# Kernel tuning notes

Hardware: AMD Instinct MI355X
Metric: run time of the kernel (lower is better)

Reference implementation:

```python
import jax, jax.numpy as jnp
import numpy as np

VOCAB, EMB, HID = 32000, 128, 128
B, S = 8, 1024


def setup_inputs() -> dict:
    key = jax.random.key(0)
    ks = jax.random.split(key, 8)
    scale_e = 1.0  # nn.Embedding default N(0,1)
    k_rnn = 1.0 / np.sqrt(HID)  # nn.RNN uniform(-1/sqrt(H), 1/sqrt(H))
    k_fc = 1.0 / np.sqrt(HID)
    return {
        "x": jax.random.randint(ks[0], (B, S), 0, VOCAB),
        "emb_table": jax.random.normal(ks[1], (VOCAB, EMB), dtype=jnp.float32) * scale_e,
        "W_ih": jax.random.uniform(ks[2], (HID, EMB), jnp.float32, -k_rnn, k_rnn),
        "b_ih": jax.random.uniform(ks[3], (HID,), jnp.float32, -k_rnn, k_rnn),
        "W_hh": jax.random.uniform(ks[4], (HID, HID), jnp.float32, -k_rnn, k_rnn),
        "b_hh": jax.random.uniform(ks[5], (HID,), jnp.float32, -k_rnn, k_rnn),
        "fc_W": jax.random.uniform(ks[6], (VOCAB, HID), jnp.float32, -k_fc, k_fc),
        "fc_b": jax.random.uniform(ks[7], (VOCAB,), jnp.float32, -k_fc, k_fc),
    }


def reference(x, emb_table, W_ih, b_ih, W_hh, b_hh, fc_W, fc_b):
    # Embedding lookup: [B,S,E]
    e = emb_table[x]
    # Precompute input projection for all timesteps: [B,S,H]
    x_proj = jnp.einsum("bse,he->bsh", e, W_ih) + b_ih + b_hh

    h0 = jnp.zeros((x.shape[0], W_hh.shape[0]), dtype=e.dtype)

    def step(h, xp_t):  # xp_t: [B,H]
        h_new = jnp.tanh(xp_t + h @ W_hh.T)
        return h_new, h_new

    # scan over time: xs [S,B,H]
    h_last, hs = jax.lax.scan(step, h0, jnp.swapaxes(x_proj, 0, 1))
    outputs = jnp.swapaxes(hs, 0, 1)  # [B,S,H]
    logits = jnp.einsum("bsh,vh->bsv", outputs, fc_W) + fc_b  # [B,S,V]
    hidden_state = h_last[None]  # [1,B,H] matching torch num_layers dim
    return logits, hidden_state
```

## Files before the change

kernel.cpp:

```cpp
#include <hip/hip_runtime.h>
#include <hip/hip_bf16.h>

#define VOCAB 32000
#define EMB   128
#define HID   128
#define BB    8
#define SS    1024

typedef __bf16 bf16x8_t __attribute__((ext_vector_type(8)));
typedef float  f32x4_t  __attribute__((ext_vector_type(4)));

__device__ __forceinline__ float dpp_xor1(float x) {
    return __int_as_float(__builtin_amdgcn_update_dpp(
        0, __float_as_int(x), 0xB1, 0xF, 0xF, true));
}
__device__ __forceinline__ float dpp_xor2(float x) {
    return __int_as_float(__builtin_amdgcn_update_dpp(
        0, __float_as_int(x), 0x4E, 0xF, 0xF, true));
}

__global__ __launch_bounds__(512) void xproj_kernel(
    const int* __restrict__ x, const float* __restrict__ emb,
    const float* __restrict__ W_ih, const float* __restrict__ b_ih,
    const float* __restrict__ b_hh, float* __restrict__ xp)
{
    const int t  = threadIdx.x;
    const int h  = t >> 2;
    const int ks = t & 3;

    float w[32];
    {
        const float* wr = W_ih + h * EMB + ks * 32;
        #pragma unroll
        for (int i = 0; i < 32; i += 4) {
            float4 v = *(const float4*)(wr + i);
            w[i] = v.x; w[i+1] = v.y; w[i+2] = v.z; w[i+3] = v.w;
        }
    }
    const float bias = b_ih[h] + b_hh[h];

    __shared__ float el[2][EMB];
    const int base = blockIdx.x * 32;

    float4 v = make_float4(0.f, 0.f, 0.f, 0.f);
    if (t < 32) v = *(const float4*)(emb + (size_t)x[base] * EMB + t * 4);

    for (int r = 0; r < 32; ++r) {
        if (t < 32) *(float4*)(&el[r & 1][t * 4]) = v;
        __syncthreads();
        if (t < 32 && r + 1 < 32)
            v = *(const float4*)(emb + (size_t)x[base + r + 1] * EMB + t * 4);

        float a0 = 0.f, a1 = 0.f, a2 = 0.f, a3 = 0.f;
        const float* e = &el[r & 1][ks * 32];
        #pragma unroll
        for (int c = 0; c < 8; ++c) {
            float4 hv = *(const float4*)(e + c * 4);
            a0 = fmaf(w[c*4+0], hv.x, a0);
            a1 = fmaf(w[c*4+1], hv.y, a1);
            a2 = fmaf(w[c*4+2], hv.z, a2);
            a3 = fmaf(w[c*4+3], hv.w, a3);
        }
        float sum = (a0 + a1) + (a2 + a3);
        sum += __shfl_xor(sum, 1);
        sum += __shfl_xor(sum, 2);
        if (ks == 0) xp[(size_t)(base + r) * HID + h] = bias + sum;
    }
}

__global__ __launch_bounds__(256) void convert_bf16_kernel(
    const float* __restrict__ in, __hip_bfloat16* __restrict__ out)
{
    const size_t i = ((size_t)blockIdx.x * 256 + threadIdx.x) * 8;
    float4 a = *(const float4*)(in + i);
    float4 b = *(const float4*)(in + i + 4);
    union { __hip_bfloat16 h[8]; uint4 u; } p;
    p.h[0] = __float2bfloat16(a.x); p.h[1] = __float2bfloat16(a.y);
    p.h[2] = __float2bfloat16(a.z); p.h[3] = __float2bfloat16(a.w);
    p.h[4] = __float2bfloat16(b.x); p.h[5] = __float2bfloat16(b.y);
    p.h[6] = __float2bfloat16(b.z); p.h[7] = __float2bfloat16(b.w);
    *(uint4*)(out + i) = p.u;
}

__global__ __launch_bounds__(256) void mega_kernel(
    const float* __restrict__ xp, const float* __restrict__ W_hh,
    __hip_bfloat16* __restrict__ hs_bf16, float* __restrict__ hidden_out,
    const __hip_bfloat16* __restrict__ Wb, const float* __restrict__ fc_b,
    float* __restrict__ C, unsigned int* __restrict__ prog)
{
    const int bid = blockIdx.x;

    if (bid < BB) {
        const int b  = bid;
        const int t  = threadIdx.x;
        const int w  = t >> 6;
        const int l  = t & 63;
        const int ks = l & 3;
        const int g  = l >> 2;
        const int jb = w * 16 + g;

        f32x4_t wr[2][8];
        #pragma unroll
        for (int m = 0; m < 2; ++m) {
            const float* src = W_hh + (size_t)(jb + 64 * m) * HID + ks * 32;
            #pragma unroll
            for (int i = 0; i < 8; ++i) wr[m][i] = *(const f32x4_t*)(src + i * 4);
        }

        __shared__ float hbuf[2][160];
        if (t < 160) hbuf[0][t] = 0.f;

        const float* xpb = xp + (size_t)b * SS * HID;
        const bool  wrt  = (ks == 0);
        const int rbase = ks * 40;

        float xsA[8][2], xsB[8][2];
        if (wrt) {
            #pragma unroll
            for (int u = 0; u < 8; ++u) {
                xsA[u][0] = xpb[(size_t)u * HID + jb];
                xsA[u][1] = xpb[(size_t)u * HID + jb + 64];
            }
        }
        __syncthreads();

#define RNN_SUPERSTEP(XC, XN, BASE)                                          \
    {                                                                        \
        const int nbase_ = (BASE) + 8;                                       \
        if (wrt && nbase_ < SS) {                                            \
            _Pragma("unroll")                                                \
            for (int u = 0; u < 8; ++u) {                                    \
                XN[u][0] = xpb[(size_t)(nbase_ + u) * HID + jb];             \
                XN[u][1] = xpb[(size_t)(nbase_ + u) * HID + jb + 64];        \
            }                                                                \
        }                                                                    \
        _Pragma("unroll")                                                    \
        for (int u = 0; u < 8; ++u) {                                        \
            const int step_ = (BASE) + u;                                    \
            const float* hc_ = hbuf[u & 1];                                  \
            f32x4_t hv[8];                                                   \
            _Pragma("unroll")                                                \
            for (int i = 0; i < 4; ++i)                                      \
                hv[i] = *(const f32x4_t*)(hc_ + rbase + i * 4);              \
            _Pragma("unroll")                                                \
            for (int i = 4; i < 8; ++i)                                      \
                hv[i] = *(const f32x4_t*)(hc_ + rbase + 4 + i * 4);          \
            f32x4_t a0 = {0.f,0.f,0.f,0.f}, a1 = a0, c0 = a0, c1 = a0;       \
            _Pragma("unroll")                                                \
            for (int i = 0; i < 4; ++i) {                                    \
                a0 += wr[0][i]   * hv[i];                                    \
                a1 += wr[0][i+4] * hv[i+4];                                  \
                c0 += wr[1][i]   * hv[i];                                    \
                c1 += wr[1][i+4] * hv[i+4];                                  \
            }                                                                \
            f32x4_t av = a0 + a1, cv = c0 + c1;                              \
            float s0 = (av.x + av.y) + (av.z + av.w);                        \
            float s1 = (cv.x + cv.y) + (cv.z + cv.w);                        \
            s0 += dpp_xor1(s0);  s0 += dpp_xor2(s0);                         \
            s1 += dpp_xor1(s1);  s1 += dpp_xor2(s1);                         \
            if (wrt) {                                                       \
                const float z0 = XC[u][0] + s0;                              \
                const float e0 = __expf(2.0f * z0);                          \
                const float h0 = 1.0f - 2.0f * __builtin_amdgcn_rcpf(e0 + 1.0f); \
                const float z1 = XC[u][1] + s1;                              \
                const float e1 = __expf(2.0f * z1);                          \
                const float h1 = 1.0f - 2.0f * __builtin_amdgcn_rcpf(e1 + 1.0f); \
                const int j0 = jb, j1 = jb + 64;                             \
                hbuf[(u + 1) & 1][j0 + ((j0 >> 4) << 2)] = h0;               \
                hbuf[(u + 1) & 1][j1 + ((j1 >> 4) << 2)] = h1;               \
                hs_bf16[((size_t)b * SS + step_) * HID + j0] = __float2bfloat16(h0); \
                hs_bf16[((size_t)b * SS + step_) * HID + j1] = __float2bfloat16(h1); \
                if (step_ == SS - 1) {                                       \
                    hidden_out[b * HID + j0] = h0;                           \
                    hidden_out[b * HID + j1] = h1;                           \
                }                                                            \
            }                                                                \
            asm volatile("s_waitcnt lgkmcnt(0)" ::: "memory");               \
            __builtin_amdgcn_s_barrier();                                    \
        }                                                                    \
    }

        for (int chunk = 0; chunk < 8; ++chunk) {
            for (int sb2 = 0; sb2 < 8; ++sb2) {
                const int base = chunk * 128 + sb2 * 16;
                RNN_SUPERSTEP(xsA, xsB, base);
                RNN_SUPERSTEP(xsB, xsA, base + 8);
            }
            asm volatile("s_waitcnt vmcnt(0)" ::: "memory");
            __builtin_amdgcn_s_barrier();
            if (t == 0)
                __hip_atomic_store(&prog[b * 16], (unsigned)(chunk + 1),
                                   __ATOMIC_RELEASE, __HIP_MEMORY_SCOPE_AGENT);
        }
#undef RNN_SUPERSTEP
    } else {
        const int cid  = bid - BB;
        const int NC   = 256 - BB;
        const int t    = threadIdx.x;
        const int lane = t & 63;
        const int cw   = t >> 6;
        const int wm   = cw >> 1;
        const int wn   = cw & 1;
        const int lr   = lane & 15;
        const int kq   = lane >> 4;

        for (int tc = 0; tc < 8; ++tc) {
            if (t == 0) {
                for (int b2 = 0; b2 < BB; ++b2) {
                    while (__hip_atomic_fetch_add(&prog[b2 * 16], 0u,
                               __ATOMIC_RELAXED, __HIP_MEMORY_SCOPE_AGENT)
                           < (unsigned)(tc + 1))
                        __builtin_amdgcn_s_sleep(32);
                }
            }
            __syncthreads();
            __builtin_amdgcn_fence(__ATOMIC_ACQUIRE, "agent");

            for (int i = cid; i < 2000; i += NC) {
                const int b2 = i / 250;
                const int nb = i % 250;
                const int mb = b2 * 8 + tc;
                const int m0 = mb * 128 + wm * 64;
                const int n0 = nb * 128 + wn * 64;

                const __hip_bfloat16* Arow = hs_bf16 + (size_t)(m0 + lr) * HID + kq * 8;
                const __hip_bfloat16* Wrow = Wb      + (size_t)(n0 + lr) * HID + kq * 8;

                f32x4_t acc[4][4];
                #pragma unroll
                for (int ii = 0; ii < 4; ++ii)
                    #pragma unroll
                    for (int jj = 0; jj < 4; ++jj)
                        acc[ii][jj] = (f32x4_t){0.f, 0.f, 0.f, 0.f};

                bf16x8_t af[2][4], bw[2][4];
                #pragma unroll
                for (int mt = 0; mt < 4; ++mt)
                    af[0][mt] = *(const bf16x8_t*)(Arow + mt * 16 * HID);
                #pragma unroll
                for (int nt = 0; nt < 4; ++nt)
                    bw[0][nt] = *(const bf16x8_t*)(Wrow + nt * 16 * HID);

                #pragma unroll
                for (int kk = 0; kk < 4; ++kk) {
                    const int cur = kk & 1, nxt = cur ^ 1;
                    if (kk < 3) {
                        const int off = (kk + 1) * 32;
                        #pragma unroll
                        for (int mt = 0; mt < 4; ++mt)
                            af[nxt][mt] = *(const bf16x8_t*)(Arow + mt * 16 * HID + off);
                        #pragma unroll
                        for (int nt = 0; nt < 4; ++nt)
                            bw[nxt][nt] = *(const bf16x8_t*)(Wrow + nt * 16 * HID + off);
                    }
                    #pragma unroll
                    for (int mt = 0; mt < 4; ++mt)
                        #pragma unroll
                        for (int nt = 0; nt < 4; ++nt)
                            acc[mt][nt] = __builtin_amdgcn_mfma_f32_16x16x32_bf16(
                                bw[cur][nt], af[cur][mt], acc[mt][nt], 0, 0, 0);
                }

                const int vq = kq * 4;
                #pragma unroll
                for (int nt = 0; nt < 4; ++nt) {
                    const int v0 = n0 + nt * 16 + vq;
                    float4 fb = *(const float4*)(fc_b + v0);
                    const f32x4_t fbv = {fb.x, fb.y, fb.z, fb.w};
                    #pragma unroll
                    for (int mt = 0; mt < 4; ++mt) {
                        const int row = m0 + mt * 16 + lr;
                        *(f32x4_t*)(C + (size_t)row * VOCAB + v0) = acc[mt][nt] + fbv;
                    }
                }
            }
        }
    }
}

extern "C" void kernel_launch(void* const* d_in, const int* in_sizes, int n_in,
                              void* d_out, int out_size, void* d_ws, size_t ws_size,
                              hipStream_t stream)
{
    const int*   x    = (const int*)  d_in[0];
    const float* emb  = (const float*)d_in[1];
    const float* W_ih = (const float*)d_in[2];
    const float* b_ih = (const float*)d_in[3];
    const float* W_hh = (const float*)d_in[4];
    const float* b_hh = (const float*)d_in[5];
    const float* fc_W = (const float*)d_in[6];
    const float* fc_b = (const float*)d_in[7];

    float* logits = (float*)d_out;
    float* hidden = logits + (size_t)BB * SS * VOCAB;

    char* ws = (char*)d_ws;
    float*           xpb = (float*)ws;
    __hip_bfloat16*  hsb = (__hip_bfloat16*)(ws + 4194304);
    __hip_bfloat16*  fwb = (__hip_bfloat16*)(ws + 6291456);
    unsigned int*    prg = (unsigned int*)(ws + 14483456);

    hipMemsetAsync(prg, 0, 1024, stream);
    xproj_kernel<<<dim3(256), dim3(512), 0, stream>>>(x, emb, W_ih, b_ih, b_hh, xpb);
    convert_bf16_kernel<<<dim3(2000), dim3(256), 0, stream>>>(fc_W, fwb);
    mega_kernel<<<dim3(256), dim3(256), 0, stream>>>(xpb, W_hh, hsb, hidden,
                                                     fwb, fc_b, logits, prg);
}
```

Baseline: 567.9 us.

## Batch all eight RNN sequences into one block using bf16 MFMA recurrence

The recurrence used to run as eight blocks, one per batch element, each doing fp32 dot products with DPP reductions. It now runs in a single block that computes h @ W_hh^T for all batch rows at once with 16x16x32 bf16 MFMA. The batch rows fill the MFMA N dimension, padded to 16 and masked. Hidden state is kept in bf16 in shared memory, and the consumer blocks poll a single progress flag instead of eight. This cuts per-step instruction latency on the serial critical path, but rounding W_hh and h to bf16 inside the recurrence may accumulate error over 1024 steps. Blocks 1-7 now sit idle.

```diff
diff --git a/kernel.cpp b/kernel.cpp
--- a/kernel.cpp
+++ b/kernel.cpp
@@ -9,15 +9,6 @@
 
 typedef __bf16 bf16x8_t __attribute__((ext_vector_type(8)));
 typedef float  f32x4_t  __attribute__((ext_vector_type(4)));
-
-__device__ __forceinline__ float dpp_xor1(float x) {
-    return __int_as_float(__builtin_amdgcn_update_dpp(
-        0, __float_as_int(x), 0xB1, 0xF, 0xF, true));
-}
-__device__ __forceinline__ float dpp_xor2(float x) {
-    return __int_as_float(__builtin_amdgcn_update_dpp(
-        0, __float_as_int(x), 0x4E, 0xF, 0xF, true));
-}
 
 __global__ __launch_bounds__(512) void xproj_kernel(
     const int* __restrict__ x, const float* __restrict__ emb,
@@ -88,115 +79,141 @@
     const __hip_bfloat16* __restrict__ Wb, const float* __restrict__ fc_b,
     float* __restrict__ C, unsigned int* __restrict__ prog)
 {
+    __shared__ __hip_bfloat16 Hb[2][2176];
+
     const int bid = blockIdx.x;
-
-    if (bid < BB) {
-        const int b  = bid;
-        const int t  = threadIdx.x;
-        const int w  = t >> 6;
+    const int t   = threadIdx.x;
+
+    if (bid == 0) {
+        const int wv = t >> 6;
         const int l  = t & 63;
-        const int ks = l & 3;
-        const int g  = l >> 2;
-        const int jb = w * 16 + g;
-
-        f32x4_t wr[2][8];
+        const int lr = l & 15;
+        const int kq = l >> 4;
+        const int j0 = (wv * 2) * 16 + kq * 4;
+        const int j1 = (wv * 2 + 1) * 16 + kq * 4;
+
+        bf16x8_t wf[2][4];
         #pragma unroll
-        for (int m = 0; m < 2; ++m) {
-            const float* src = W_hh + (size_t)(jb + 64 * m) * HID + ks * 32;
+        for (int mt = 0; mt < 2; ++mt) {
+            const float* wr = W_hh + (size_t)((wv * 2 + mt) * 16 + lr) * HID + kq * 8;
             #pragma unroll
-            for (int i = 0; i < 8; ++i) wr[m][i] = *(const f32x4_t*)(src + i * 4);
-        }
-
-        __shared__ float hbuf[2][160];
-        if (t < 160) hbuf[0][t] = 0.f;
-
-        const float* xpb = xp + (size_t)b * SS * HID;
-        const bool  wrt  = (ks == 0);
-        const int rbase = ks * 40;
-
-        float xsA[8][2], xsB[8][2];
-        if (wrt) {
+            for (int kf = 0; kf < 4; ++kf) {
+                float4 u0 = *(const float4*)(wr + kf * 32);
+                float4 u1 = *(const float4*)(wr + kf * 32 + 4);
+                union { __hip_bfloat16 q[8]; bf16x8_t v; } pk;
+                pk.q[0] = __float2bfloat16(u0.x); pk.q[1] = __float2bfloat16(u0.y);
+                pk.q[2] = __float2bfloat16(u0.z); pk.q[3] = __float2bfloat16(u0.w);
+                pk.q[4] = __float2bfloat16(u1.x); pk.q[5] = __float2bfloat16(u1.y);
+                pk.q[6] = __float2bfloat16(u1.z); pk.q[7] = __float2bfloat16(u1.w);
+                wf[mt][kf] = pk.v;
+            }
+        }
+
+        {
+            __hip_bfloat16* hb = &Hb[0][0];
+            for (int i = t; i < 2 * 2176; i += 256) hb[i] = __float2bfloat16(0.f);
+        }
+
+        const float*          xpL = xp      + (size_t)lr * SS * HID;
+        __hip_bfloat16*       hsL = hs_bf16 + (size_t)lr * SS * HID;
+        const int  hoff = lr * 136 + kq * 8;
+        const bool act  = (lr < 8);
+
+        float4 xsA[2][2], xsB[2][2];
+        if (act) {
             #pragma unroll
-            for (int u = 0; u < 8; ++u) {
-                xsA[u][0] = xpb[(size_t)u * HID + jb];
-                xsA[u][1] = xpb[(size_t)u * HID + jb + 64];
+            for (int u = 0; u < 2; ++u) {
+                xsA[u][0] = *(const float4*)(xpL + (size_t)u * HID + j0);
+                xsA[u][1] = *(const float4*)(xpL + (size_t)u * HID + j1);
             }
         }
         __syncthreads();
 
-#define RNN_SUPERSTEP(XC, XN, BASE)                                          \
+#define PSTEP(XC, u, stepi)                                                  \
     {                                                                        \
-        const int nbase_ = (BASE) + 8;                                       \
-        if (wrt && nbase_ < SS) {                                            \
-            _Pragma("unroll")                                                \
-            for (int u = 0; u < 8; ++u) {                                    \
-                XN[u][0] = xpb[(size_t)(nbase_ + u) * HID + jb];             \
-                XN[u][1] = xpb[(size_t)(nbase_ + u) * HID + jb + 64];        \
+        const __hip_bfloat16* hc = &Hb[(stepi) & 1][0];                      \
+        bf16x8_t hf0 = *(const bf16x8_t*)(hc + hoff);                        \
+        bf16x8_t hf1 = *(const bf16x8_t*)(hc + hoff + 32);                   \
+        bf16x8_t hf2 = *(const bf16x8_t*)(hc + hoff + 64);                   \
+        bf16x8_t hf3 = *(const bf16x8_t*)(hc + hoff + 96);                   \
+        f32x4_t ac0 = {0.f, 0.f, 0.f, 0.f}, ac1 = ac0;                       \
+        ac0 = __builtin_amdgcn_mfma_f32_16x16x32_bf16(wf[0][0], hf0, ac0, 0, 0, 0); \
+        ac1 = __builtin_amdgcn_mfma_f32_16x16x32_bf16(wf[1][0], hf0, ac1, 0, 0, 0); \
+        ac0 = __builtin_amdgcn_mfma_f32_16x16x32_bf16(wf[0][1], hf1, ac0, 0, 0, 0); \
+        ac1 = __builtin_amdgcn_mfma_f32_16x16x32_bf16(wf[1][1], hf1, ac1, 0, 0, 0); \
+        ac0 = __builtin_amdgcn_mfma_f32_16x16x32_bf16(wf[0][2], hf2, ac0, 0, 0, 0); \
+        ac1 = __builtin_amdgcn_mfma_f32_16x16x32_bf16(wf[1][2], hf2, ac1, 0, 0, 0); \
+        ac0 = __builtin_amdgcn_mfma_f32_16x16x32_bf16(wf[0][3], hf3, ac0, 0, 0, 0); \
+        ac1 = __builtin_amdgcn_mfma_f32_16x16x32_bf16(wf[1][3], hf3, ac1, 0, 0, 0); \
+        if (act) {                                                           \
+            const float4 xc0 = XC[u][0], xc1 = XC[u][1];                     \
+            float z, ee;                                                     \
+            z = xc0.x + ac0[0]; ee = __expf(2.f * z);                        \
+            const float h00 = 1.f - 2.f * __builtin_amdgcn_rcpf(ee + 1.f);   \
+            z = xc0.y + ac0[1]; ee = __expf(2.f * z);                        \
+            const float h01 = 1.f - 2.f * __builtin_amdgcn_rcpf(ee + 1.f);   \
+            z = xc0.z + ac0[2]; ee = __expf(2.f * z);                        \
+            const float h02 = 1.f - 2.f * __builtin_amdgcn_rcpf(ee + 1.f);   \
+            z = xc0.w + ac0[3]; ee = __expf(2.f * z);                        \
+            const float h03 = 1.f - 2.f * __builtin_amdgcn_rcpf(ee + 1.f);   \
+            z = xc1.x + ac1[0]; ee = __expf(2.f * z);                        \
+            const float h10 = 1.f - 2.f * __builtin_amdgcn_rcpf(ee + 1.f);   \
+            z = xc1.y + ac1[1]; ee = __expf(2.f * z);                        \
+            const float h11 = 1.f - 2.f * __builtin_amdgcn_rcpf(ee + 1.f);   \
+            z = xc1.z + ac1[2]; ee = __expf(2.f * z);                        \
+            const float h12 = 1.f - 2.f * __builtin_amdgcn_rcpf(ee + 1.f);   \
+            z = xc1.w + ac1[3]; ee = __expf(2.f * z);                        \
+            const float h13 = 1.f - 2.f * __builtin_amdgcn_rcpf(ee + 1.f);   \
+            union { __hip_bfloat16 q[4]; uint2 u2; } p0, p1;                 \
+            p0.q[0] = __float2bfloat16(h00); p0.q[1] = __float2bfloat16(h01);\
+            p0.q[2] = __float2bfloat16(h02); p0.q[3] = __float2bfloat16(h03);\
+            p1.q[0] = __float2bfloat16(h10); p1.q[1] = __float2bfloat16(h11);\
+            p1.q[2] = __float2bfloat16(h12); p1.q[3] = __float2bfloat16(h13);\
+            *(uint2*)(&Hb[((stepi) + 1) & 1][lr * 136 + j0]) = p0.u2;        \
+            *(uint2*)(&Hb[((stepi) + 1) & 1][lr * 136 + j1]) = p1.u2;        \
+            *(uint2*)(hsL + (size_t)(stepi) * HID + j0) = p0.u2;             \
+            *(uint2*)(hsL + (size_t)(stepi) * HID + j1) = p1.u2;             \
+            if ((stepi) == SS - 1) {                                         \
+                *(float4*)(hidden_out + lr * HID + j0) =                     \
+                    make_float4(h00, h01, h02, h03);                         \
+                *(float4*)(hidden_out + lr * HID + j1) =                     \
+                    make_float4(h10, h11, h12, h13);                         \
             }                                                                \
         }                                                                    \
-        _Pragma("unroll")                                                    \
-        for (int u = 0; u < 8; ++u) {                                        \
-            const int step_ = (BASE) + u;                                    \
-            const float* hc_ = hbuf[u & 1];                                  \
-            f32x4_t hv[8];                                                   \
+        asm volatile("s_waitcnt lgkmcnt(0)" ::: "memory");                   \
+        __builtin_amdgcn_s_barrier();                                        \
+    }
+
+#define SUPER2(XC, XN, BASE)                                                 \
+    {                                                                        \
+        if (act && (BASE) + 3 < SS) {                                        \
             _Pragma("unroll")                                                \
-            for (int i = 0; i < 4; ++i)                                      \
-                hv[i] = *(const f32x4_t*)(hc_ + rbase + i * 4);              \
-            _Pragma("unroll")                                                \
-            for (int i = 4; i < 8; ++i)                                      \
-                hv[i] = *(const f32x4_t*)(hc_ + rbase + 4 + i * 4);          \
-            f32x4_t a0 = {0.f,0.f,0.f,0.f}, a1 = a0, c0 = a0, c1 = a0;       \
-            _Pragma("unroll")                                                \
-            for (int i = 0; i < 4; ++i) {                                    \
-                a0 += wr[0][i]   * hv[i];                                    \
-                a1 += wr[0][i+4] * hv[i+4];                                  \
-                c0 += wr[1][i]   * hv[i];                                    \
-                c1 += wr[1][i+4] * hv[i+4];                                  \
+            for (int u = 0; u < 2; ++u) {                                    \
+                XN[u][0] = *(const float4*)(xpL + (size_t)((BASE) + 2 + u) * HID + j0); \
+                XN[u][1] = *(const float4*)(xpL + (size_t)((BASE) + 2 + u) * HID + j1); \
             }                                                                \
-            f32x4_t av = a0 + a1, cv = c0 + c1;                              \
-            float s0 = (av.x + av.y) + (av.z + av.w);                        \
-            float s1 = (cv.x + cv.y) + (cv.z + cv.w);                        \
-            s0 += dpp_xor1(s0);  s0 += dpp_xor2(s0);                         \
-            s1 += dpp_xor1(s1);  s1 += dpp_xor2(s1);                         \
-            if (wrt) {                                                       \
-                const float z0 = XC[u][0] + s0;                              \
-                const float e0 = __expf(2.0f * z0);                          \
-                const float h0 = 1.0f - 2.0f * __builtin_amdgcn_rcpf(e0 + 1.0f); \
-                const float z1 = XC[u][1] + s1;                              \
-                const float e1 = __expf(2.0f * z1);                          \
-                const float h1 = 1.0f - 2.0f * __builtin_amdgcn_rcpf(e1 + 1.0f); \
-                const int j0 = jb, j1 = jb + 64;                             \
-                hbuf[(u + 1) & 1][j0 + ((j0 >> 4) << 2)] = h0;               \
-                hbuf[(u + 1) & 1][j1 + ((j1 >> 4) << 2)] = h1;               \
-                hs_bf16[((size_t)b * SS + step_) * HID + j0] = __float2bfloat16(h0); \
-                hs_bf16[((size_t)b * SS + step_) * HID + j1] = __float2bfloat16(h1); \
-                if (step_ == SS - 1) {                                       \
-                    hidden_out[b * HID + j0] = h0;                           \
-                    hidden_out[b * HID + j1] = h1;                           \
-                }                                                            \
-            }                                                                \
-            asm volatile("s_waitcnt lgkmcnt(0)" ::: "memory");               \
-            __builtin_amdgcn_s_barrier();                                    \
         }                                                                    \
+        PSTEP(XC, 0, (BASE))                                                 \
+        PSTEP(XC, 1, (BASE) + 1)                                             \
     }
 
         for (int chunk = 0; chunk < 8; ++chunk) {
-            for (int sb2 = 0; sb2 < 8; ++sb2) {
-                const int base = chunk * 128 + sb2 * 16;
-                RNN_SUPERSTEP(xsA, xsB, base);
-                RNN_SUPERSTEP(xsB, xsA, base + 8);
+            for (int sb = 0; sb < 32; ++sb) {
+                const int base = chunk * 128 + sb * 4;
+                SUPER2(xsA, xsB, base);
+                SUPER2(xsB, xsA, base + 2);
             }
             asm volatile("s_waitcnt vmcnt(0)" ::: "memory");
             __builtin_amdgcn_s_barrier();
             if (t == 0)
-                __hip_atomic_store(&prog[b * 16], (unsigned)(chunk + 1),
+                __hip_atomic_store(&prog[0], (unsigned)(chunk + 1),
                                    __ATOMIC_RELEASE, __HIP_MEMORY_SCOPE_AGENT);
         }
-#undef RNN_SUPERSTEP
-    } else {
+#undef SUPER2
+#undef PSTEP
+    } else if (bid >= BB) {
         const int cid  = bid - BB;
         const int NC   = 256 - BB;
-        const int t    = threadIdx.x;
         const int lane = t & 63;
         const int cw   = t >> 6;
         const int wm   = cw >> 1;
@@ -206,12 +223,10 @@
 
         for (int tc = 0; tc < 8; ++tc) {
             if (t == 0) {
-                for (int b2 = 0; b2 < BB; ++b2) {
-                    while (__hip_atomic_fetch_add(&prog[b2 * 16], 0u,
-                               __ATOMIC_RELAXED, __HIP_MEMORY_SCOPE_AGENT)
-                           < (unsigned)(tc + 1))
-                        __builtin_amdgcn_s_sleep(32);
-                }
+                while (__hip_atomic_fetch_add(&prog[0], 0u,
+                           __ATOMIC_RELAXED, __HIP_MEMORY_SCOPE_AGENT)
+                       < (unsigned)(tc + 1))
+                    __builtin_amdgcn_s_sleep(32);
             }
             __syncthreads();
             __builtin_amdgcn_fence(__ATOMIC_ACQUIRE, "agent");
```

Result: slower. 877.7 us (+54.6%).
